# Performance work log

Hardware: AMD Instinct MI355X
Metric: run time of the kernel (lower is better)

## Reference

```python
import jax, jax.numpy as jnp
import numpy as np

N_IM, N_OBJ = 16, 16          # images, objects per image
D_IN = 2048                    # obj_pair_feat_dim
PER_IM = N_OBJ * (N_OBJ + 1) // 2   # obj boxes + union boxes per image
N_BOX = N_IM * PER_IM               # 2176
N_PAIR = N_IM * N_OBJ * (N_OBJ - 1) # is_ex=True -> 2*C(n,2) per image = 3840
NUM_REL = 3


def setup_inputs() -> dict:
    rng = np.random.default_rng(0)
    H, W = 600.0, 800.0
    boxes = np.zeros((N_BOX, 5), np.float32)
    o1i, o2i, ui, imi = [], [], [], []
    for i in range(N_IM):
        off = i * PER_IM
        x1 = rng.uniform(0, W / 2, N_OBJ); y1 = rng.uniform(0, H / 2, N_OBJ)
        bw = rng.uniform(10, W / 2, N_OBJ); bh = rng.uniform(10, H / 2, N_OBJ)
        boxes[off:off + N_OBJ] = np.stack([np.full(N_OBJ, i), x1, y1, x1 + bw, y1 + bh], 1)
        uc = off + N_OBJ
        for a in range(N_OBJ):
            for b in range(a + 1, N_OBJ):
                boxes[uc] = [i, min(x1[a], x1[b]), min(y1[a], y1[b]),
                             max(x1[a] + bw[a], x1[b] + bw[b]), max(y1[a] + bh[a], y1[b] + bh[b])]
                o1i += [off + a, off + b]; o2i += [off + b, off + a]
                ui += [uc, uc]; imi += [i, i]
                uc += 1
    im_info = np.tile(np.array([H, W, 1.0], np.float32), (N_IM, 1))
    key = jax.random.key(0)
    ks = jax.random.split(key, 16)
    lin = lambda k, i, o: jax.random.normal(k, (i, o), jnp.float32) * 0.02
    return dict(
        xs=jax.random.normal(ks[0], (N_PAIR, D_IN), jnp.float32) * 0.1,
        xo=jax.random.normal(ks[1], (N_PAIR, D_IN), jnp.float32) * 0.1,
        xu=jax.random.normal(ks[2], (N_PAIR, D_IN), jnp.float32) * 0.1,
        boxes=jnp.asarray(boxes), im_info=jnp.asarray(im_info),
        o1_idx=jnp.asarray(o1i, jnp.int32), o2_idx=jnp.asarray(o2i, jnp.int32),
        u_idx=jnp.asarray(ui, jnp.int32), img_idx=jnp.asarray(imi, jnp.int32),
        Ws1=lin(ks[3], D_IN, 512), bs1=jnp.zeros(512, jnp.float32),
        Ws2=lin(ks[4], 512, 256), bs2=jnp.zeros(256, jnp.float32),
        Wo1=lin(ks[5], D_IN, 512), bo1=jnp.zeros(512, jnp.float32),
        Wo2=lin(ks[6], 512, 256), bo2=jnp.zeros(256, jnp.float32),
        Wu1=lin(ks[7], D_IN, 512), bu1=jnp.zeros(512, jnp.float32),
        Wu2=lin(ks[8], 512, 256), bu2=jnp.zeros(256, jnp.float32),
        Wc1=lin(ks[9], 256 + 19, 256), bc1=jnp.zeros(256, jnp.float32),
        Wc2=lin(ks[10], 256, NUM_REL), bc2=jnp.zeros(NUM_REL, jnp.float32),
    )


def _mlp(x, W1, b1, W2, b2):
    return jax.nn.relu(jax.nn.relu(x @ W1 + b1) @ W2 + b2)


def _encode_loc(sb, ob, ub, hw):
    # sb/ob/ub: [P,4] (x1,y1,x2,y2); hw: [P,2] (h_i, w_i)
    h_i, w_i = hw[:, 0], hw[:, 1]
    x_s = (sb[:, 0] + sb[:, 2]) / 2.0; y_s = (sb[:, 1] + sb[:, 3]) / 2.0
    w_s = sb[:, 2] - sb[:, 0]; h_s = sb[:, 3] - sb[:, 1]
    x_o = (ob[:, 0] + ob[:, 2]) / 2.0; y_o = (ob[:, 1] + ob[:, 3]) / 2.0
    w_o = ob[:, 2] - ob[:, 0]; h_o = ob[:, 3] - ob[:, 1]
    a_s = w_s * h_s; a_o = w_o * h_o
    a_u = (ub[:, 2] - ub[:, 0]) * (ub[:, 3] - ub[:, 1])
    area = w_i * h_i
    return jnp.stack([
        x_s / w_i, y_s / h_i, (x_s + w_s) / w_i, (y_s + h_s) / h_i, a_s / area,
        x_o / w_i, y_o / h_i, (x_o + w_o) / w_i, (y_o + h_o) / h_i, a_o / area,
        (x_s - x_o) / w_o, (y_s - y_o) / h_o, jnp.log(w_s / w_o), jnp.log(h_s / h_o),
        (x_o - x_s) / w_s, (y_o - y_s) / h_s, jnp.log(w_o / w_s), jnp.log(h_o / h_s),
        a_u / area], axis=1)  # [P,19]


def reference(xs, xo, xu, boxes, im_info, o1_idx, o2_idx, u_idx, img_idx,
              Ws1, bs1, Ws2, bs2, Wo1, bo1, Wo2, bo2, Wu1, bu1, Wu2, bu2,
              Wc1, bc1, Wc2, bc2):
    fs = _mlp(xs, Ws1, bs1, Ws2, bs2)
    fo = _mlp(xo, Wo1, bo1, Wo2, bo2)
    fu = _mlp(xu, Wu1, bu1, Wu2, bu2)
    appear = fu - fo - fs                              # [P,256]
    loc = _encode_loc(boxes[o1_idx, 1:5], boxes[o2_idx, 1:5],
                      boxes[u_idx, 1:5], im_info[img_idx, :2])  # [P,19]
    h = jax.nn.relu(jnp.concatenate([appear, loc], axis=1) @ Wc1 + bc1)
    return h @ Wc2 + bc2                               # [P,num_rel]
```

## Files before the change

kernel.cpp:

```cpp
#include <hip/hip_runtime.h>

#define N_PAIR 3840

typedef short bf16x8 __attribute__((ext_vector_type(8)));
typedef float f32x4 __attribute__((ext_vector_type(4)));

static __device__ __forceinline__ ushort f2bf(float f) {
    uint x = __float_as_uint(f);
    uint r = (x + 0x7FFFu + ((x >> 16) & 1u)) >> 16;
    return (ushort)r;
}
static __device__ __forceinline__ float bf2f(ushort u) {
    return __uint_as_float(((uint)u) << 16);
}

#define GLOAD16(GP, LP)                                                        \
    __builtin_amdgcn_global_load_lds(                                          \
        (const __attribute__((address_space(1))) void*)(GP),                   \
        (__attribute__((address_space(3))) void*)(LP), 16, 0, 0)

__global__ void transpose_convert(const float* __restrict__ in0,
                                  const float* __restrict__ in1,
                                  const float* __restrict__ in2,
                                  ushort* __restrict__ out,
                                  int K, int N, int Kpad) {
    const float* in = (blockIdx.z == 0) ? in0 : (blockIdx.z == 1 ? in1 : in2);
    ushort* o = out + (size_t)blockIdx.z * N * Kpad;
    __shared__ float tile[64][65];
    int k0 = blockIdx.x * 64, n0 = blockIdx.y * 64;
    int t = threadIdx.x;
    int r = t >> 2, c4 = (t & 3) * 16;
#pragma unroll
    for (int i = 0; i < 16; i++) {
        int k = k0 + r, n = n0 + c4 + i;
        tile[r][c4 + i] = (k < K && n < N) ? in[(size_t)k * N + n] : 0.f;
    }
    __syncthreads();
#pragma unroll
    for (int i = 0; i < 16; i++) {
        int n = n0 + r, k = k0 + c4 + i;
        if (n < N && k < Kpad) o[(size_t)n * Kpad + k] = f2bf(tile[c4 + i][r]);
    }
}

__global__ void transpose_convert2(const float* __restrict__ Ws2,
                                   const float* __restrict__ Wo2,
                                   const float* __restrict__ Wu2,
                                   const float* __restrict__ Wc1,
                                   ushort* __restrict__ W2T,
                                   ushort* __restrict__ WC1T) {
    int z = blockIdx.z;
    const float* in; ushort* o; int K, N, Kpad;
    if (z < 3) {
        in = (z == 0) ? Ws2 : (z == 1 ? Wo2 : Wu2);
        o = W2T + (size_t)z * 256 * 512; K = 512; N = 256; Kpad = 512;
    } else {
        in = Wc1; o = WC1T; K = 275; N = 256; Kpad = 288;
    }
    __shared__ float tile[64][65];
    int k0 = blockIdx.x * 64, n0 = blockIdx.y * 64;
    int t = threadIdx.x;
    int r = t >> 2, c4 = (t & 3) * 16;
#pragma unroll
    for (int i = 0; i < 16; i++) {
        int k = k0 + r, n = n0 + c4 + i;
        tile[r][c4 + i] = (k < K && n < N) ? in[(size_t)k * N + n] : 0.f;
    }
    __syncthreads();
#pragma unroll
    for (int i = 0; i < 16; i++) {
        int n = n0 + r, k = k0 + c4 + i;
        if (n < N && k < Kpad) o[(size_t)n * Kpad + k] = f2bf(tile[c4 + i][r]);
    }
}

__device__ __forceinline__ bf16x8 frag_ld(const ushort* __restrict__ lds, int row, int colbyte) {
    int off = (row << 7) + (colbyte ^ ((row & 7) << 4));
    return *reinterpret_cast<const bf16x8*>(reinterpret_cast<const char*>(lds) + off);
}
__device__ __forceinline__ bf16x8 frag32_ld(const ushort* __restrict__ lds, int row, int colbyte) {
    int off = (row << 6) + (colbyte ^ ((row & 3) << 4));
    return *reinterpret_cast<const bf16x8*>(reinterpret_cast<const char*>(lds) + off);
}

__global__ __launch_bounds__(256) void gemm1(const float* __restrict__ xs,
                                             const float* __restrict__ xo,
                                             const float* __restrict__ xu,
                                             const ushort* __restrict__ w1t,
                                             const float* __restrict__ b_s,
                                             const float* __restrict__ b_o,
                                             const float* __restrict__ b_u,
                                             ushort* __restrict__ h1out) {
    int bid = blockIdx.x;
    int w = (bid & 7) * 90 + (bid >> 3);
    int br = w / 240; int r = w - br * 240;
    int xt = r >> 2, yt = r & 3;

    const float* x = br == 0 ? xs : (br == 1 ? xo : xu);
    const ushort* wt = w1t + (size_t)br * 512 * 2048;
    const float* bias = br == 0 ? b_s : (br == 1 ? b_o : b_u);
    ushort* out = h1out + (size_t)br * 3840 * 512;

    __shared__ ushort As[2][64 * 64];
    __shared__ ushort Bs[2][128 * 64];
    int t = threadIdx.x, lane = t & 63, wid = t >> 6;
    int wr = wid >> 1, wc = wid & 1;
    int m0 = xt * 64, n0 = yt * 128;
    const float* asrc = x + (size_t)m0 * 2048;
    const ushort* bsrc = wt + (size_t)n0 * 2048;

    int ar = t >> 2, ac = (t & 3) * 16;
    float4 pa[4];

#define G1_AISSUE(KT)                                                                     \
    {                                                                                     \
        const float4* g = reinterpret_cast<const float4*>(asrc + (size_t)ar * 2048 + (KT) + ac); \
        pa[0] = g[0]; pa[1] = g[1]; pa[2] = g[2]; pa[3] = g[3];                           \
    }
#define G1_ACOMMIT(BUF)                                                                   \
    {                                                                                     \
        union { bf16x8 v; ushort us[8]; } p0, p1;                                         \
        _Pragma("unroll")                                                                 \
        for (int i = 0; i < 4; i++) {                                                     \
            p0.us[i] = f2bf(pa[0][i]); p0.us[4 + i] = f2bf(pa[1][i]);                     \
            p1.us[i] = f2bf(pa[2][i]); p1.us[4 + i] = f2bf(pa[3][i]);                     \
        }                                                                                 \
        char* ab = reinterpret_cast<char*>(&As[BUF][0]);                                  \
        int off0 = (ar << 7) + ((ac << 1) ^ ((ar & 7) << 4));                             \
        int off1 = (ar << 7) + (((ac + 8) << 1) ^ ((ar & 7) << 4));                       \
        *reinterpret_cast<bf16x8*>(ab + off0) = p0.v;                                     \
        *reinterpret_cast<bf16x8*>(ab + off1) = p1.v;                                     \
    }
#define G1_BGLOAD(BUF, KT)                                                                \
    {                                                                                     \
        _Pragma("unroll")                                                                 \
        for (int it = 0; it < 4; it++) {                                                  \
            int g = (wid * 4 + it) * 64 + lane;                                           \
            int rr = g >> 3, cc = g & 7;                                                  \
            const ushort* gp = bsrc + (size_t)rr * 2048 + (KT) + ((cc ^ (rr & 7)) << 3);  \
            ushort* lp = &Bs[BUF][g * 8];                                                 \
            GLOAD16(gp, lp);                                                              \
        }                                                                                 \
    }
#define G1_MFMA(BUF)                                                                      \
    _Pragma("unroll")                                                                     \
    for (int kk = 0; kk < 64; kk += 32) {                                                 \
        int cb = (kk + ((lane >> 4) << 3)) << 1;                                          \
        bf16x8 a[2], b[4];                                                                \
        _Pragma("unroll")                                                                 \
        for (int i = 0; i < 2; i++) a[i] = frag_ld(&As[BUF][0], wr * 32 + i * 16 + (lane & 15), cb); \
        _Pragma("unroll")                                                                 \
        for (int f = 0; f < 4; f++) b[f] = frag_ld(&Bs[BUF][0], wc * 64 + f * 16 + (lane & 15), cb); \
        _Pragma("unroll")                                                                 \
        for (int i = 0; i < 2; i++)                                                       \
            _Pragma("unroll")                                                             \
            for (int j = 0; j < 4; j++)                                                   \
                acc[i][j] = __builtin_amdgcn_mfma_f32_16x16x32_bf16(a[i], b[j], acc[i][j], 0, 0, 0); \
    }

    f32x4 acc[2][4] = {};
    G1_AISSUE(0)
    G1_BGLOAD(0, 0)
    G1_ACOMMIT(0)
    __syncthreads();
    int cur = 0;
    for (int kt = 0; kt < 2048; kt += 64) {
        if (kt + 64 < 2048) {
            G1_BGLOAD(cur ^ 1, kt + 64)
            G1_AISSUE(kt + 64)
        }
        G1_MFMA(cur)
        if (kt + 64 < 2048) G1_ACOMMIT(cur ^ 1)
        __syncthreads();
        cur ^= 1;
    }
    int rb = m0 + wr * 32 + ((lane >> 4) << 2);
    int cb0 = n0 + wc * 64 + (lane & 15);
#pragma unroll
    for (int j = 0; j < 4; j++) {
        int col = cb0 + j * 16;
        float bv = bias[col];
#pragma unroll
        for (int i = 0; i < 2; i++)
#pragma unroll
            for (int q = 0; q < 4; q++) {
                int row = rb + i * 16 + q;
                float v = acc[i][j][q] + bv;
                v = v > 0.f ? v : 0.f;
                out[(size_t)row * 512 + col] = f2bf(v);
            }
    }
#undef G1_AISSUE
#undef G1_ACOMMIT
#undef G1_BGLOAD
#undef G1_MFMA
}

__global__ __launch_bounds__(256) void gemm2(const ushort* __restrict__ h1,
                                             const ushort* __restrict__ w2t,
                                             const float* __restrict__ b_s,
                                             const float* __restrict__ b_o,
                                             const float* __restrict__ b_u,
                                             ushort* __restrict__ h2br) {
    int bid = blockIdx.x;
    int w = (bid & 7) * 45 + (bid >> 3);
    int br = w / 120; int r = w - br * 120;
    int xt = r >> 1, yt = r & 1;

    const ushort* A = h1 + (size_t)br * 3840 * 512;
    const ushort* B = w2t + (size_t)br * 256 * 512;
    const float* bias = br == 0 ? b_s : (br == 1 ? b_o : b_u);
    ushort* out = h2br + (size_t)br * 3840 * 256;

    __shared__ ushort As[2][64 * 64];
    __shared__ ushort Bs[2][128 * 64];
    int t = threadIdx.x, lane = t & 63, wid = t >> 6;
    int wr = wid >> 1, wc = wid & 1;
    int m0 = xt * 64, n0 = yt * 128;
    const ushort* asrc = A + (size_t)m0 * 512;
    const ushort* bsrc = B + (size_t)n0 * 512;

#define G2_GLOADS(BUF, KT)                                                                \
    {                                                                                     \
        _Pragma("unroll")                                                                 \
        for (int it = 0; it < 2; it++) {                                                  \
            int g = (wid * 2 + it) * 64 + lane;                                           \
            int rr = g >> 3, cc = g & 7;                                                  \
            const ushort* gp = asrc + (size_t)rr * 512 + (KT) + ((cc ^ (rr & 7)) << 3);   \
            GLOAD16(gp, &As[BUF][g * 8]);                                                 \
        }                                                                                 \
        _Pragma("unroll")                                                                 \
        for (int it = 0; it < 4; it++) {                                                  \
            int g = (wid * 4 + it) * 64 + lane;                                           \
            int rr = g >> 3, cc = g & 7;                                                  \
            const ushort* gp = bsrc + (size_t)rr * 512 + (KT) + ((cc ^ (rr & 7)) << 3);   \
            GLOAD16(gp, &Bs[BUF][g * 8]);                                                 \
        }                                                                                 \
    }
#define G2_MFMA(BUF)                                                                      \
    _Pragma("unroll")                                                                     \
    for (int kk = 0; kk < 64; kk += 32) {                                                 \
        int cb = (kk + ((lane >> 4) << 3)) << 1;                                          \
        bf16x8 a[2], b[4];                                                                \
        _Pragma("unroll")                                                                 \
        for (int i = 0; i < 2; i++) a[i] = frag_ld(&As[BUF][0], wr * 32 + i * 16 + (lane & 15), cb); \
        _Pragma("unroll")                                                                 \
        for (int f = 0; f < 4; f++) b[f] = frag_ld(&Bs[BUF][0], wc * 64 + f * 16 + (lane & 15), cb); \
        _Pragma("unroll")                                                                 \
        for (int i = 0; i < 2; i++)                                                       \
            _Pragma("unroll")                                                             \
            for (int j = 0; j < 4; j++)                                                   \
                acc[i][j] = __builtin_amdgcn_mfma_f32_16x16x32_bf16(a[i], b[j], acc[i][j], 0, 0, 0); \
    }

    f32x4 acc[2][4] = {};
    G2_GLOADS(0, 0)
    __syncthreads();
    int cur = 0;
    for (int kt = 0; kt < 512; kt += 64) {
        if (kt + 64 < 512) G2_GLOADS(cur ^ 1, kt + 64)
        G2_MFMA(cur)
        __syncthreads();
        cur ^= 1;
    }
    int rb = m0 + wr * 32 + ((lane >> 4) << 2);
    int cb0 = n0 + wc * 64 + (lane & 15);
#pragma unroll
    for (int j = 0; j < 4; j++) {
        int col = cb0 + j * 16;
        float bv = bias[col];
#pragma unroll
        for (int i = 0; i < 2; i++)
#pragma unroll
            for (int q = 0; q < 4; q++) {
                int row = rb + i * 16 + q;
                float v = acc[i][j][q] + bv;
                v = v > 0.f ? v : 0.f;
                out[(size_t)row * 256 + col] = f2bf(v);
            }
    }
#undef G2_GLOADS
#undef G2_MFMA
}

__global__ void appear_pack(const ushort* __restrict__ h2br,
                            ushort* __restrict__ hin,
                            const float* __restrict__ boxes,
                            const float* __restrict__ im_info,
                            const int* __restrict__ o1, const int* __restrict__ o2,
                            const int* __restrict__ u, const int* __restrict__ im) {
    int i = blockIdx.x * 256 + threadIdx.x;
    if (i < N_PAIR * 32) {
        int p = i >> 5, ch = (i & 31) * 8;
        const ushort* ps = h2br + (size_t)p * 256 + ch;
        bf16x8 vs = *reinterpret_cast<const bf16x8*>(ps);
        bf16x8 vo = *reinterpret_cast<const bf16x8*>(ps + (size_t)3840 * 256);
        bf16x8 vu = *reinterpret_cast<const bf16x8*>(ps + (size_t)2 * 3840 * 256);
        union { bf16x8 v; ushort us[8]; } r;
#pragma unroll
        for (int j = 0; j < 8; j++)
            r.us[j] = f2bf(bf2f(((ushort)vu[j])) - bf2f(((ushort)vo[j])) - bf2f(((ushort)vs[j])));
        *reinterpret_cast<bf16x8*>(hin + (size_t)p * 288 + ch) = r.v;
    }
    if (blockIdx.x < 15) {
        int p = blockIdx.x * 256 + threadIdx.x;
        const float* sb = boxes + 5 * o1[p] + 1;
        const float* ob = boxes + 5 * o2[p] + 1;
        const float* ub = boxes + 5 * u[p] + 1;
        const float* ii = im_info + 3 * im[p];
        float hi = ii[0], wi = ii[1];
        float x_s = (sb[0] + sb[2]) * 0.5f, y_s = (sb[1] + sb[3]) * 0.5f;
        float w_s = sb[2] - sb[0], h_s = sb[3] - sb[1];
        float x_o = (ob[0] + ob[2]) * 0.5f, y_o = (ob[1] + ob[3]) * 0.5f;
        float w_o = ob[2] - ob[0], h_o = ob[3] - ob[1];
        float a_s = w_s * h_s, a_o = w_o * h_o;
        float a_u = (ub[2] - ub[0]) * (ub[3] - ub[1]);
        float area = wi * hi;
        float f[19];
        f[0] = x_s / wi;            f[1] = y_s / hi;
        f[2] = (x_s + w_s) / wi;    f[3] = (y_s + h_s) / hi;
        f[4] = a_s / area;
        f[5] = x_o / wi;            f[6] = y_o / hi;
        f[7] = (x_o + w_o) / wi;    f[8] = (y_o + h_o) / hi;
        f[9] = a_o / area;
        f[10] = (x_s - x_o) / w_o;  f[11] = (y_s - y_o) / h_o;
        f[12] = logf(w_s / w_o);    f[13] = logf(h_s / h_o);
        f[14] = (x_o - x_s) / w_s;  f[15] = (y_o - y_s) / h_s;
        f[16] = logf(w_o / w_s);    f[17] = logf(h_o / h_s);
        f[18] = a_u / area;
        ushort* row = hin + (size_t)p * 288 + 256;
#pragma unroll
        for (int k = 0; k < 19; k++) row[k] = f2bf(f[k]);
#pragma unroll
        for (int k = 19; k < 32; k++) row[k] = 0;
    }
}

__global__ __launch_bounds__(256) void gemm3(const ushort* __restrict__ hin,
                                             const ushort* __restrict__ wc1t,
                                             const float* __restrict__ bc1,
                                             ushort* __restrict__ h2) {
    __shared__ ushort As[2][64 * 32];
    __shared__ ushort Bs[2][128 * 32];
    int t = threadIdx.x, lane = t & 63, wid = t >> 6;
    int wr = wid >> 1, wc = wid & 1;
    int m0 = blockIdx.x * 64, n0 = blockIdx.y * 128;
    const ushort* asrc = hin + (size_t)m0 * 288;
    const ushort* bsrc = wc1t + (size_t)n0 * 288;

    int ar = t >> 2, ac = (t & 3) * 8;
    bf16x8 pa, pb[2];
    auto issue = [&](int kt) {
        pa = *reinterpret_cast<const bf16x8*>(asrc + (size_t)ar * 288 + kt + ac);
#pragma unroll
        for (int it = 0; it < 2; it++) {
            int e = (it * 256 + t) * 8;
            int rr = e >> 5, cc = e & 31;
            pb[it] = *reinterpret_cast<const bf16x8*>(bsrc + (size_t)rr * 288 + kt + cc);
        }
    };
    auto commit = [&](int buf) {
        char* ab = reinterpret_cast<char*>(&As[buf][0]);
        int off0 = (ar << 6) + ((ac << 1) ^ ((ar & 3) << 4));
        *reinterpret_cast<bf16x8*>(ab + off0) = pa;
        char* bb = reinterpret_cast<char*>(&Bs[buf][0]);
#pragma unroll
        for (int it = 0; it < 2; it++) {
            int e = (it * 256 + t) * 8;
            int rr = e >> 5, cc = e & 31;
            int off = (rr << 6) + ((cc << 1) ^ ((rr & 3) << 4));
            *reinterpret_cast<bf16x8*>(bb + off) = pb[it];
        }
    };

    f32x4 acc[2][4] = {};
    issue(0);
    commit(0);
    __syncthreads();
    int cur = 0;
    for (int kt = 0; kt < 288; kt += 32) {
        int nxt = kt + 32;
        if (nxt < 288) issue(nxt);
        int cb = ((lane >> 4) << 3) << 1;
        bf16x8 a[2], b[4];
#pragma unroll
        for (int i = 0; i < 2; i++) a[i] = frag32_ld(&As[cur][0], wr * 32 + i * 16 + (lane & 15), cb);
#pragma unroll
        for (int f = 0; f < 4; f++) b[f] = frag32_ld(&Bs[cur][0], wc * 64 + f * 16 + (lane & 15), cb);
#pragma unroll
        for (int i = 0; i < 2; i++)
#pragma unroll
            for (int j = 0; j < 4; j++)
                acc[i][j] = __builtin_amdgcn_mfma_f32_16x16x32_bf16(a[i], b[j], acc[i][j], 0, 0, 0);
        if (nxt < 288) commit(cur ^ 1);
        __syncthreads();
        cur ^= 1;
    }
    int rb = m0 + wr * 32 + ((lane >> 4) << 2);
    int cb0 = n0 + wc * 64 + (lane & 15);
#pragma unroll
    for (int j = 0; j < 4; j++) {
        int col = cb0 + j * 16;
        float bv = bc1[col];
#pragma unroll
        for (int i = 0; i < 2; i++)
#pragma unroll
            for (int q = 0; q < 4; q++) {
                int row = rb + i * 16 + q;
                float v = acc[i][j][q] + bv;
                v = v > 0.f ? v : 0.f;
                h2[(size_t)row * 256 + col] = f2bf(v);
            }
    }
}

__global__ void final_fc(const ushort* __restrict__ h2,
                         const float* __restrict__ wc2,
                         const float* __restrict__ bc2,
                         float* __restrict__ out) {
    __shared__ float w[768];
    int t = threadIdx.x;
    for (int i = t; i < 768; i += 256) w[i] = wc2[i];
    __syncthreads();
    int g = t >> 4, l = t & 15;
    int row = blockIdx.x * 16 + g;
    const ushort* hr = h2 + (size_t)row * 256 + l * 16;
    bf16x8 v0 = *reinterpret_cast<const bf16x8*>(hr);
    bf16x8 v1 = *reinterpret_cast<const bf16x8*>(hr + 8);
    float s0 = 0.f, s1 = 0.f, s2 = 0.f;
#pragma unroll
    for (int k = 0; k < 8; k++) {
        float h = bf2f((ushort)v0[k]);
        int c = (l * 16 + k) * 3;
        s0 += h * w[c]; s1 += h * w[c + 1]; s2 += h * w[c + 2];
    }
#pragma unroll
    for (int k = 0; k < 8; k++) {
        float h = bf2f((ushort)v1[k]);
        int c = (l * 16 + 8 + k) * 3;
        s0 += h * w[c]; s1 += h * w[c + 1]; s2 += h * w[c + 2];
    }
#pragma unroll
    for (int m = 1; m < 16; m <<= 1) {
        s0 += __shfl_xor(s0, m);
        s1 += __shfl_xor(s1, m);
        s2 += __shfl_xor(s2, m);
    }
    if (l == 0) {
        out[row * 3 + 0] = s0 + bc2[0];
        out[row * 3 + 1] = s1 + bc2[1];
        out[row * 3 + 2] = s2 + bc2[2];
    }
}

extern "C" void kernel_launch(void* const* d_in, const int* in_sizes, int n_in,
                              void* d_out, int out_size, void* d_ws, size_t ws_size,
                              hipStream_t stream) {
    (void)in_sizes; (void)n_in; (void)out_size; (void)ws_size;
    const float* xs = (const float*)d_in[0];
    const float* xo = (const float*)d_in[1];
    const float* xu = (const float*)d_in[2];
    const float* boxes = (const float*)d_in[3];
    const float* im_info = (const float*)d_in[4];
    const int* o1 = (const int*)d_in[5];
    const int* o2 = (const int*)d_in[6];
    const int* uu = (const int*)d_in[7];
    const int* im = (const int*)d_in[8];
    const float* Ws1 = (const float*)d_in[9];
    const float* bs1 = (const float*)d_in[10];
    const float* Ws2 = (const float*)d_in[11];
    const float* bs2 = (const float*)d_in[12];
    const float* Wo1 = (const float*)d_in[13];
    const float* bo1 = (const float*)d_in[14];
    const float* Wo2 = (const float*)d_in[15];
    const float* bo2 = (const float*)d_in[16];
    const float* Wu1 = (const float*)d_in[17];
    const float* bu1 = (const float*)d_in[18];
    const float* Wu2 = (const float*)d_in[19];
    const float* bu2 = (const float*)d_in[20];
    const float* Wc1 = (const float*)d_in[21];
    const float* bc1 = (const float*)d_in[22];
    const float* Wc2 = (const float*)d_in[23];
    const float* bc2 = (const float*)d_in[24];
    float* out = (float*)d_out;

    ushort* W1T = (ushort*)d_ws;
    ushort* H2BR = W1T;
    ushort* W2T = W1T + (size_t)3 * 512 * 2048;
    ushort* WC1T = W2T + (size_t)3 * 256 * 512;
    ushort* H1 = WC1T + (size_t)256 * 288;
    ushort* HIN = H1 + (size_t)3 * 3840 * 512;
    ushort* H2 = HIN + (size_t)3840 * 288;

    transpose_convert<<<dim3(32, 8, 3), 256, 0, stream>>>(Ws1, Wo1, Wu1, W1T, 2048, 512, 2048);
    transpose_convert2<<<dim3(8, 4, 4), 256, 0, stream>>>(Ws2, Wo2, Wu2, Wc1, W2T, WC1T);
    gemm1<<<720, 256, 0, stream>>>(xs, xo, xu, W1T, bs1, bo1, bu1, H1);
    gemm2<<<360, 256, 0, stream>>>(H1, W2T, bs2, bo2, bu2, H2BR);
    appear_pack<<<480, 256, 0, stream>>>(H2BR, HIN, boxes, im_info, o1, o2, uu, im);
    gemm3<<<dim3(60, 2), 256, 0, stream>>>(HIN, WC1T, bc1, H2);
    final_fc<<<240, 256, 0, stream>>>(H2, Wc2, bc2, out);
}
```

Baseline: 99.98 us.

## Split-K gemm1 with larger 128x128 tiles and separate bias/ReLU reduction

```diff
diff --git a/kernel.cpp b/kernel.cpp
--- a/kernel.cpp
+++ b/kernel.cpp
@@ -83,117 +83,114 @@
     return *reinterpret_cast<const bf16x8*>(reinterpret_cast<const char*>(lds) + off);
 }
 
-__global__ __launch_bounds__(256) void gemm1(const float* __restrict__ xs,
-                                             const float* __restrict__ xo,
-                                             const float* __restrict__ xu,
-                                             const ushort* __restrict__ w1t,
-                                             const float* __restrict__ b_s,
-                                             const float* __restrict__ b_o,
-                                             const float* __restrict__ b_u,
-                                             ushort* __restrict__ h1out) {
+__global__ __launch_bounds__(256) void gemm1_main(const float* __restrict__ xs,
+                                                  const float* __restrict__ xo,
+                                                  const float* __restrict__ xu,
+                                                  const ushort* __restrict__ w1t,
+                                                  float* __restrict__ part) {
     int bid = blockIdx.x;
     int w = (bid & 7) * 90 + (bid >> 3);
     int br = w / 240; int r = w - br * 240;
-    int xt = r >> 2, yt = r & 3;
+    int mt = r >> 3, nt = (r >> 1) & 3, ks = r & 1;
 
     const float* x = br == 0 ? xs : (br == 1 ? xo : xu);
     const ushort* wt = w1t + (size_t)br * 512 * 2048;
-    const float* bias = br == 0 ? b_s : (br == 1 ? b_o : b_u);
-    ushort* out = h1out + (size_t)br * 3840 * 512;
-
-    __shared__ ushort As[2][64 * 64];
-    __shared__ ushort Bs[2][128 * 64];
+    float* out = part + ((size_t)(ks * 3 + br)) * 3840 * 512;
+
+    __shared__ ushort As[128 * 64];
+    __shared__ ushort Bs[128 * 64];
     int t = threadIdx.x, lane = t & 63, wid = t >> 6;
     int wr = wid >> 1, wc = wid & 1;
-    int m0 = xt * 64, n0 = yt * 128;
-    const float* asrc = x + (size_t)m0 * 2048;
-    const ushort* bsrc = wt + (size_t)n0 * 2048;
-
-    int ar = t >> 2, ac = (t & 3) * 16;
-    float4 pa[4];
-
-#define G1_AISSUE(KT)                                                                     \
-    {                                                                                     \
-        const float4* g = reinterpret_cast<const float4*>(asrc + (size_t)ar * 2048 + (KT) + ac); \
-        pa[0] = g[0]; pa[1] = g[1]; pa[2] = g[2]; pa[3] = g[3];                           \
-    }
-#define G1_ACOMMIT(BUF)                                                                   \
-    {                                                                                     \
-        union { bf16x8 v; ushort us[8]; } p0, p1;                                         \
-        _Pragma("unroll")                                                                 \
-        for (int i = 0; i < 4; i++) {                                                     \
-            p0.us[i] = f2bf(pa[0][i]); p0.us[4 + i] = f2bf(pa[1][i]);                     \
-            p1.us[i] = f2bf(pa[2][i]); p1.us[4 + i] = f2bf(pa[3][i]);                     \
-        }                                                                                 \
-        char* ab = reinterpret_cast<char*>(&As[BUF][0]);                                  \
-        int off0 = (ar << 7) + ((ac << 1) ^ ((ar & 7) << 4));                             \
-        int off1 = (ar << 7) + (((ac + 8) << 1) ^ ((ar & 7) << 4));                       \
-        *reinterpret_cast<bf16x8*>(ab + off0) = p0.v;                                     \
-        *reinterpret_cast<bf16x8*>(ab + off1) = p1.v;                                     \
-    }
-#define G1_BGLOAD(BUF, KT)                                                                \
-    {                                                                                     \
-        _Pragma("unroll")                                                                 \
-        for (int it = 0; it < 4; it++) {                                                  \
-            int g = (wid * 4 + it) * 64 + lane;                                           \
-            int rr = g >> 3, cc = g & 7;                                                  \
-            const ushort* gp = bsrc + (size_t)rr * 2048 + (KT) + ((cc ^ (rr & 7)) << 3);  \
-            ushort* lp = &Bs[BUF][g * 8];                                                 \
-            GLOAD16(gp, lp);                                                              \
-        }                                                                                 \
-    }
-#define G1_MFMA(BUF)                                                                      \
-    _Pragma("unroll")                                                                     \
-    for (int kk = 0; kk < 64; kk += 32) {                                                 \
-        int cb = (kk + ((lane >> 4) << 3)) << 1;                                          \
-        bf16x8 a[2], b[4];                                                                \
-        _Pragma("unroll")                                                                 \
-        for (int i = 0; i < 2; i++) a[i] = frag_ld(&As[BUF][0], wr * 32 + i * 16 + (lane & 15), cb); \
-        _Pragma("unroll")                                                                 \
-        for (int f = 0; f < 4; f++) b[f] = frag_ld(&Bs[BUF][0], wc * 64 + f * 16 + (lane & 15), cb); \
-        _Pragma("unroll")                                                                 \
-        for (int i = 0; i < 2; i++)                                                       \
-            _Pragma("unroll")                                                             \
-            for (int j = 0; j < 4; j++)                                                   \
-                acc[i][j] = __builtin_amdgcn_mfma_f32_16x16x32_bf16(a[i], b[j], acc[i][j], 0, 0, 0); \
-    }
-
-    f32x4 acc[2][4] = {};
-    G1_AISSUE(0)
-    G1_BGLOAD(0, 0)
-    G1_ACOMMIT(0)
-    __syncthreads();
-    int cur = 0;
-    for (int kt = 0; kt < 2048; kt += 64) {
-        if (kt + 64 < 2048) {
-            G1_BGLOAD(cur ^ 1, kt + 64)
-            G1_AISSUE(kt + 64)
+    int m0 = mt * 128, n0 = nt * 128, k0 = ks * 1024;
+    const float* asrc = x + (size_t)m0 * 2048 + k0;
+    const ushort* bsrc = wt + (size_t)n0 * 2048 + k0;
+
+    int ar = t >> 1, ac = (t & 1) * 32;
+
+    f32x4 acc[4][4] = {};
+    for (int kt = 0; kt < 1024; kt += 64) {
+        __syncthreads();
+#pragma unroll
+        for (int it = 0; it < 4; it++) {
+            int g = (wid * 4 + it) * 64 + lane;
+            int rr = g >> 3, cc = g & 7;
+            const ushort* gp = bsrc + (size_t)rr * 2048 + kt + ((cc ^ (rr & 7)) << 3);
+            GLOAD16(gp, &Bs[g * 8]);
         }
-        G1_MFMA(cur)
-        if (kt + 64 < 2048) G1_ACOMMIT(cur ^ 1)
+        {
+            const float4* g = reinterpret_cast<const float4*>(asrc + (size_t)ar * 2048 + kt + ac);
+            float4 v0 = g[0], v1 = g[1], v2 = g[2], v3 = g[3];
+            float4 v4 = g[4], v5 = g[5], v6 = g[6], v7 = g[7];
+            char* ab = reinterpret_cast<char*>(&As[0]);
+            union { bf16x8 v; ushort us[8]; } pk;
+#pragma unroll
+            for (int i = 0; i < 4; i++) { pk.us[i] = f2bf(v0[i]); pk.us[4 + i] = f2bf(v1[i]); }
+            *reinterpret_cast<bf16x8*>(ab + ((ar << 7) + (((ac + 0) << 1) ^ ((ar & 7) << 4)))) = pk.v;
+#pragma unroll
+            for (int i = 0; i < 4; i++) { pk.us[i] = f2bf(v2[i]); pk.us[4 + i] = f2bf(v3[i]); }
+            *reinterpret_cast<bf16x8*>(ab + ((ar << 7) + (((ac + 8) << 1) ^ ((ar & 7) << 4)))) = pk.v;
+#pragma unroll
+            for (int i = 0; i < 4; i++) { pk.us[i] = f2bf(v4[i]); pk.us[4 + i] = f2bf(v5[i]); }
+            *reinterpret_cast<bf16x8*>(ab + ((ar << 7) + (((ac + 16) << 1) ^ ((ar & 7) << 4)))) = pk.v;
+#pragma unroll
+            for (int i = 0; i < 4; i++) { pk.us[i] = f2bf(v6[i]); pk.us[4 + i] = f2bf(v7[i]); }
+            *reinterpret_cast<bf16x8*>(ab + ((ar << 7) + (((ac + 24) << 1) ^ ((ar & 7) << 4)))) = pk.v;
+        }
         __syncthreads();
-        cur ^= 1;
-    }
-    int rb = m0 + wr * 32 + ((lane >> 4) << 2);
+#pragma unroll
+        for (int kk = 0; kk < 64; kk += 32) {
+            int cb = (kk + ((lane >> 4) << 3)) << 1;
+            bf16x8 a[4], b[4];
+#pragma unroll
+            for (int i = 0; i < 4; i++) a[i] = frag_ld(&As[0], wr * 64 + i * 16 + (lane & 15), cb);
+#pragma unroll
+            for (int f = 0; f < 4; f++) b[f] = frag_ld(&Bs[0], wc * 64 + f * 16 + (lane & 15), cb);
+#pragma unroll
+            for (int i = 0; i < 4; i++)
+#pragma unroll
+                for (int j = 0; j < 4; j++)
+                    acc[i][j] = __builtin_amdgcn_mfma_f32_16x16x32_bf16(a[i], b[j], acc[i][j], 0, 0, 0);
+        }
+    }
+    int rb = m0 + wr * 64 + ((lane >> 4) << 2);
     int cb0 = n0 + wc * 64 + (lane & 15);
 #pragma unroll
     for (int j = 0; j < 4; j++) {
         int col = cb0 + j * 16;
-        float bv = bias[col];
-#pragma unroll
-        for (int i = 0; i < 2; i++)
-#pragma unroll
-            for (int q = 0; q < 4; q++) {
-                int row = rb + i * 16 + q;
-                float v = acc[i][j][q] + bv;
-                v = v > 0.f ? v : 0.f;
-                out[(size_t)row * 512 + col] = f2bf(v);
-            }
-    }
-#undef G1_AISSUE
-#undef G1_ACOMMIT
-#undef G1_BGLOAD
-#undef G1_MFMA
+#pragma unroll
+        for (int i = 0; i < 4; i++)
+#pragma unroll
+            for (int q = 0; q < 4; q++)
+                out[(size_t)(rb + i * 16 + q) * 512 + col] = acc[i][j][q];
+    }
+}
+
+__global__ void reduce_h1(const float* __restrict__ part,
+                          const float* __restrict__ bs1,
+                          const float* __restrict__ bo1,
+                          const float* __restrict__ bu1,
+                          ushort* __restrict__ h1) {
+    const size_t D = (size_t)3840 * 512;
+    size_t e = ((size_t)blockIdx.x * 256 + threadIdx.x) * 8;
+    if (e >= 3 * D) return;
+    int br = (int)(e / D);
+    int col = (int)(e & 511);
+    const float* bias = br == 0 ? bs1 : (br == 1 ? bo1 : bu1);
+    const float4* p0 = reinterpret_cast<const float4*>(part + e);
+    const float4* p1 = reinterpret_cast<const float4*>(part + 3 * D + e);
+    const float4* bp = reinterpret_cast<const float4*>(bias + col);
+    float4 a0 = p0[0], a1 = p0[1];
+    float4 b0 = p1[0], b1 = p1[1];
+    float4 c0 = bp[0], c1 = bp[1];
+    union { bf16x8 v; ushort us[8]; } r;
+#pragma unroll
+    for (int i = 0; i < 4; i++) {
+        float v = a0[i] + b0[i] + c0[i];
+        r.us[i] = f2bf(v > 0.f ? v : 0.f);
+        float w = a1[i] + b1[i] + c1[i];
+        r.us[4 + i] = f2bf(w > 0.f ? w : 0.f);
+    }
+    *reinterpret_cast<bf16x8*>(h1 + e) = r.v;
 }
 
 __global__ __launch_bounds__(256) void gemm2(const ushort* __restrict__ h1,
@@ -491,10 +488,12 @@
     ushort* H1 = WC1T + (size_t)256 * 288;
     ushort* HIN = H1 + (size_t)3 * 3840 * 512;
     ushort* H2 = HIN + (size_t)3840 * 288;
+    float* PART = (float*)(H2 + (size_t)3840 * 256);
 
     transpose_convert<<<dim3(32, 8, 3), 256, 0, stream>>>(Ws1, Wo1, Wu1, W1T, 2048, 512, 2048);
     transpose_convert2<<<dim3(8, 4, 4), 256, 0, stream>>>(Ws2, Wo2, Wu2, Wc1, W2T, WC1T);
-    gemm1<<<720, 256, 0, stream>>>(xs, xo, xu, W1T, bs1, bo1, bu1, H1);
+    gemm1_main<<<720, 256, 0, stream>>>(xs, xo, xu, W1T, PART);
+    reduce_h1<<<2880, 256, 0, stream>>>(PART, bs1, bo1, bu1, H1);
     gemm2<<<360, 256, 0, stream>>>(H1, W2T, bs2, bo2, bu2, H2BR);
     appear_pack<<<480, 256, 0, stream>>>(H2BR, HIN, boxes, im_info, o1, o2, uu, im);
     gemm3<<<dim3(60, 2), 256, 0, stream>>>(HIN, WC1T, bc1, H2);
```

After: 137.2 us. +37.2%, slower.
